# Kernel optimization log

Measured on AMD Instinct MI355X. Metric: run time of the kernel, lower is better.

The kernel has to match this reference:

```python
import jax, jax.numpy as jnp
import numpy as np

E = 256   # embedding_channels
C = 128   # c
N1 = 512
N2 = 512
NE1 = 16384
NE2 = 16384
EPS = 1e-5


def _ln(x, w, b):
    m = x.mean(-1, keepdims=True)
    v = jnp.mean((x - m) ** 2, axis=-1, keepdims=True)
    return (x - m) * jax.lax.rsqrt(v + EPS) * w + b


def _lin(x, w, b):
    return x @ w.T + b


def setup_inputs() -> dict:
    key = jax.random.key(0)
    ks = jax.random.split(key, 12)
    p = lambda k, shape: jax.random.normal(k, shape, jnp.float32) * 0.02
    return {
        "z": jax.random.normal(ks[0], (N1, N2, E), jnp.float32),
        "efeat1": jax.random.normal(ks[1], (NE1, E), jnp.float32),
        "efeat2": jax.random.normal(ks[2], (NE2, E), jnp.float32),
        "ln_w": jnp.ones((E,), jnp.float32), "ln_b": jnp.zeros((E,), jnp.float32),
        "lnc_w": jnp.ones((C,), jnp.float32), "lnc_b": jnp.zeros((C,), jnp.float32),
        "gl1_w": p(ks[3], (C, E)), "gl1_b": jnp.zeros((C,), jnp.float32),
        "gl2_w": p(ks[4], (C, E)), "gl2_b": jnp.zeros((C,), jnp.float32),
        "l1_w": p(ks[5], (C, E)), "l1_b": jnp.zeros((C,), jnp.float32),
        "l2_w": p(ks[6], (C, E)), "l2_b": jnp.zeros((C,), jnp.float32),
        "eg_w": p(ks[7], (E, E)), "eg_b": jnp.zeros((E,), jnp.float32),
        "las_w": p(ks[8], (E, C)), "las_b": jnp.zeros((E,), jnp.float32),
        "edges1": jax.random.randint(ks[9], (2, NE1), 0, N1, jnp.int64 if jax.config.jax_enable_x64 else jnp.int32),
        "edges2": jax.random.randint(ks[10], (2, NE2), 0, N2, jnp.int64 if jax.config.jax_enable_x64 else jnp.int32),
    }


def reference(z, efeat1, efeat2, ln_w, ln_b, lnc_w, lnc_b, gl1_w, gl1_b,
              gl2_w, gl2_b, l1_w, l1_b, l2_w, l2_b, eg_w, eg_b,
              las_w, las_b, edges1, edges2):
    zl = _ln(z, ln_w, ln_b)                       # [n1,n2,E]
    p1 = _ln(efeat1, ln_w, ln_b)                  # [ne1,E]
    p2 = _ln(efeat2, ln_w, ln_b)                  # [ne2,E]

    gate = lambda x, gw, gb, lw, lb: jax.nn.sigmoid(_lin(x, gw, gb)) * _lin(x, lw, lb)
    ab1 = gate(zl, gl1_w, gl1_b, l1_w, l1_b)      # [n1,n2,C]
    ab2 = gate(zl, gl2_w, gl2_b, l2_w, l2_b)      # [n1,n2,C]
    p1 = gate(p1, gl1_w, gl1_b, l1_w, l1_b)       # [ne1,C]
    p2 = gate(p2, gl2_w, gl2_b, l2_w, l2_b)       # [ne2,C]
    g = jax.nn.sigmoid(_lin(zl, eg_w, eg_b))      # [n1,n2,E]

    n1, n2 = z.shape[0], z.shape[1]
    # sparse COO -> dense (duplicate indices sum, matching torch coalesce)
    P1 = jnp.zeros((n1, n1, C), z.dtype).at[edges1[0], edges1[1]].add(p1)
    P2 = jnp.zeros((n2, n2, C), z.dtype).at[edges2[0], edges2[1]].add(p2)

    block1 = jnp.einsum('ikc,kjc->ijc', P1, ab1)  # [n1,n2,C]
    block2 = jnp.einsum('ikc,jkc->ijc', ab2, P2)  # [n1,n2,C]

    return g * _lin(_ln(block1 + block2, lnc_w, lnc_b), las_w, las_b)
```

## Files before the change

kernel.cpp:

```cpp
#include <hip/hip_runtime.h>
#include <stdint.h>

#define NN 512
#define EE 256
#define CC 128
#define NEDGE 16384
#define RR (NN*NN)
#define RT3 (RR + 2*NEDGE)

using bf16x8 = __attribute__((ext_vector_type(8))) short;
using f32x4  = __attribute__((ext_vector_type(4))) float;

__device__ __forceinline__ unsigned short f2bf(float f) {
  union { float f; unsigned u; } v; v.f = f;
  unsigned r = v.u + 0x7FFFu + ((v.u >> 16) & 1u);
  return (unsigned short)(r >> 16);
}
__device__ __forceinline__ float bf2f(unsigned short h) {
  union { unsigned u; float f; } v; v.u = ((unsigned)h) << 16;
  return v.f;
}
__device__ __forceinline__ float sigm(float x) { return 1.f / (1.f + __expf(-x)); }

__global__ __launch_bounds__(256) void k_ln(
    const float* __restrict__ z, const float* __restrict__ e1,
    const float* __restrict__ e2, const float* __restrict__ lnw,
    const float* __restrict__ lnb, unsigned short* __restrict__ zl) {
  int row = blockIdx.x * 4 + (threadIdx.x >> 6);
  int lane = threadIdx.x & 63;
  const float* src;
  if (row < RR)            src = z  + (size_t)row * EE;
  else if (row < RR+NEDGE) src = e1 + (size_t)(row - RR) * EE;
  else                     src = e2 + (size_t)(row - RR - NEDGE) * EE;
  float4 v = ((const float4*)src)[lane];
  float s = v.x + v.y + v.z + v.w;
  float q = v.x*v.x + v.y*v.y + v.z*v.z + v.w*v.w;
  #pragma unroll
  for (int o = 32; o > 0; o >>= 1) { s += __shfl_xor(s, o); q += __shfl_xor(q, o); }
  float m = s * (1.f/EE);
  float rstd = rsqrtf(q*(1.f/EE) - m*m + 1e-5f);
  float4 wv = ((const float4*)lnw)[lane];
  float4 bv = ((const float4*)lnb)[lane];
  ushort4 o4;
  o4.x = f2bf((v.x - m)*rstd*wv.x + bv.x);
  o4.y = f2bf((v.y - m)*rstd*wv.y + bv.y);
  o4.z = f2bf((v.z - m)*rstd*wv.z + bv.z);
  o4.w = f2bf((v.w - m)*rstd*wv.w + bv.w);
  ((ushort4*)(zl + (size_t)row * EE))[lane] = o4;
}

__global__ __launch_bounds__(256) void k_wconv(
    const float* __restrict__ gl1, const float* __restrict__ l1,
    const float* __restrict__ gl2, const float* __restrict__ l2,
    const float* __restrict__ eg,  const float* __restrict__ las,
    unsigned short* __restrict__ Wcol, unsigned short* __restrict__ Wrow,
    unsigned short* __restrict__ Wlas) {
  int t = blockIdx.x * 256 + threadIdx.x;
  if (t < 65536) {
    Wcol[t] = f2bf(t < 32768 ? gl1[t] : l1[t - 32768]);
  } else if (t < 196608) {
    int u = t - 65536;
    float v = (u < 32768) ? gl2[u] : (u < 65536) ? l2[u - 32768] : eg[u - 65536];
    Wrow[u] = f2bf(v);
  } else {
    int u = t - 196608;
    Wlas[u] = f2bf(las[u]);
  }
}

__global__ __launch_bounds__(256) void k_proj_gate(
    const unsigned short* __restrict__ zl, const unsigned short* __restrict__ W,
    const float* __restrict__ gb, const float* __restrict__ lb,
    unsigned short* __restrict__ abOut, float* __restrict__ Pf,
    const int* __restrict__ edges, int mode) {
  __shared__ __attribute__((aligned(16))) short As[128*32];
  __shared__ __attribute__((aligned(16))) short Bg[128*32];
  __shared__ __attribute__((aligned(16))) short Bl[128*32];
  const int t = threadIdx.x, w = t >> 6, lane = t & 63;
  const int mt = blockIdx.x;
  const bool isE = (mt >= RR/128);
  size_t abase; int astride;
  if (!isE) {
    if (mode == 0) { int rt0 = mt*128; abase = (size_t)(rt0 & 511)*512 + (rt0 >> 9); astride = 512; }
    else           { abase = (size_t)mt*128; astride = 1; }
  } else {
    abase = (size_t)RR + (mode ? NEDGE : 0) + (mt*128 - RR); astride = 1;
  }
  const f32x4 z4 = {0.f, 0.f, 0.f, 0.f};
  f32x4 ag[4][4], al[4][4];
  #pragma unroll
  for (int a = 0; a < 4; ++a)
    #pragma unroll
    for (int b = 0; b < 4; ++b) { ag[a][b] = z4; al[a][b] = z4; }
  const int wr = (w >> 1)*64, wc = (w & 1)*64;
  #pragma unroll 1
  for (int kk = 0; kk < 8; ++kk) {
    const int k0 = kk * 32;
    __syncthreads();
    #pragma unroll
    for (int s2 = 0; s2 < 2; ++s2) {
      int sidx = t + s2*256, row = sidx >> 2, seg = sidx & 3;
      int lo = row*32 + seg*8;
      *(uint4*)&As[lo] = *(const uint4*)(zl + (abase + (size_t)row*astride)*EE + k0 + seg*8);
      const unsigned short* wp = W + (size_t)row*EE + k0 + seg*8;
      *(uint4*)&Bg[lo] = *(const uint4*)wp;
      *(uint4*)&Bl[lo] = *(const uint4*)(wp + 128*EE);
    }
    __syncthreads();
    bf16x8 af[4], bgf[4], blf[4];
    #pragma unroll
    for (int f = 0; f < 4; ++f) {
      af[f]  = *(const bf16x8*)&As[(wr + f*16 + (lane & 15))*32 + (lane >> 4)*8];
      bgf[f] = *(const bf16x8*)&Bg[(wc + f*16 + (lane & 15))*32 + (lane >> 4)*8];
      blf[f] = *(const bf16x8*)&Bl[(wc + f*16 + (lane & 15))*32 + (lane >> 4)*8];
    }
    #pragma unroll
    for (int fm = 0; fm < 4; ++fm)
      #pragma unroll
      for (int fn = 0; fn < 4; ++fn) {
        ag[fm][fn] = __builtin_amdgcn_mfma_f32_16x16x32_bf16(af[fm], bgf[fn], ag[fm][fn], 0, 0, 0);
        al[fm][fn] = __builtin_amdgcn_mfma_f32_16x16x32_bf16(af[fm], blf[fn], al[fm][fn], 0, 0, 0);
      }
  }
  const int quad = lane >> 4, lc = lane & 15;
  #pragma unroll
  for (int fm = 0; fm < 4; ++fm)
    #pragma unroll
    for (int fn = 0; fn < 4; ++fn) {
      int c = wc + fn*16 + lc;
      float bgv = gb[c], blv = lb[c];
      float v0 = sigm(ag[fm][fn][0] + bgv) * (al[fm][fn][0] + blv);
      float v1 = sigm(ag[fm][fn][1] + bgv) * (al[fm][fn][1] + blv);
      float v2 = sigm(ag[fm][fn][2] + bgv) * (al[fm][fn][2] + blv);
      float v3 = sigm(ag[fm][fn][3] + bgv) * (al[fm][fn][3] + blv);
      int rl = wr + fm*16 + quad*4;
      if (!isE) {
        size_t rt = (size_t)mt*128 + rl;
        ushort4 o; o.x = f2bf(v0); o.y = f2bf(v1); o.z = f2bf(v2); o.w = f2bf(v3);
        *(ushort4*)&abOut[(size_t)c*RR + rt] = o;
      } else {
        int e0 = mt*128 - RR + rl;
        float vv[4] = {v0, v1, v2, v3};
        #pragma unroll
        for (int rg = 0; rg < 4; ++rg) {
          int e = e0 + rg;
          int i0 = edges[e], i1 = edges[NEDGE + e];
          atomicAdd(&Pf[((size_t)i0*NN + i1)*CC + c], vv[rg]);
        }
      }
    }
}

__global__ __launch_bounds__(256) void k_proj_g(
    const unsigned short* __restrict__ zl, const unsigned short* __restrict__ Weg,
    const float* __restrict__ egb, unsigned short* __restrict__ gOut) {
  __shared__ __attribute__((aligned(16))) short As[128*32];
  __shared__ __attribute__((aligned(16))) short Bs[128*32];
  const int t = threadIdx.x, w = t >> 6, lane = t & 63;
  const int mt = blockIdx.x, half = blockIdx.y;
  const size_t abase = (size_t)mt * 128;
  const unsigned short* Wb = Weg + (size_t)half * 128 * EE;
  const f32x4 z4 = {0.f, 0.f, 0.f, 0.f};
  f32x4 acc[4][4];
  #pragma unroll
  for (int a = 0; a < 4; ++a)
    #pragma unroll
    for (int b = 0; b < 4; ++b) acc[a][b] = z4;
  const int wr = (w >> 1)*64, wc = (w & 1)*64;
  #pragma unroll 1
  for (int kk = 0; kk < 8; ++kk) {
    const int k0 = kk * 32;
    __syncthreads();
    #pragma unroll
    for (int s2 = 0; s2 < 2; ++s2) {
      int sidx = t + s2*256, row = sidx >> 2, seg = sidx & 3;
      int lo = row*32 + seg*8;
      *(uint4*)&As[lo] = *(const uint4*)(zl + (abase + row)*EE + k0 + seg*8);
      *(uint4*)&Bs[lo] = *(const uint4*)(Wb + (size_t)row*EE + k0 + seg*8);
    }
    __syncthreads();
    bf16x8 af[4], bf_[4];
    #pragma unroll
    for (int f = 0; f < 4; ++f) {
      af[f]  = *(const bf16x8*)&As[(wr + f*16 + (lane & 15))*32 + (lane >> 4)*8];
      bf_[f] = *(const bf16x8*)&Bs[(wc + f*16 + (lane & 15))*32 + (lane >> 4)*8];
    }
    #pragma unroll
    for (int fm = 0; fm < 4; ++fm)
      #pragma unroll
      for (int fn = 0; fn < 4; ++fn)
        acc[fm][fn] = __builtin_amdgcn_mfma_f32_16x16x32_bf16(af[fm], bf_[fn], acc[fm][fn], 0, 0, 0);
  }
  const int quad = lane >> 4, lc = lane & 15;
  #pragma unroll
  for (int fm = 0; fm < 4; ++fm)
    #pragma unroll
    for (int fn = 0; fn < 4; ++fn) {
      int e = half*128 + wc + fn*16 + lc;
      float bv = egb[e];
      size_t r0 = (size_t)mt*128 + wr + fm*16 + quad*4;
      #pragma unroll
      for (int rg = 0; rg < 4; ++rg)
        gOut[(r0 + rg)*EE + e] = f2bf(sigm(acc[fm][fn][rg] + bv));
    }
}

__global__ __launch_bounds__(256) void k_pcvt(
    const float* __restrict__ P1f, const float* __restrict__ P2f,
    unsigned short* __restrict__ P1c, unsigned short* __restrict__ P2c) {
  const float* src = blockIdx.y ? P2f : P1f;
  unsigned short* dst = blockIdx.y ? P2c : P1c;
  __shared__ float Ls[128*65];
  const int t = threadIdx.x;
  const size_t pos0 = (size_t)blockIdx.x * 64;
  #pragma unroll
  for (int it = 0; it < 8; ++it) {
    int fi = t + it*256;
    int p = fi >> 5, cq = fi & 31;
    float4 v = ((const float4*)(src + (pos0 + p)*CC))[cq];
    Ls[(cq*4+0)*65 + p] = v.x; Ls[(cq*4+1)*65 + p] = v.y;
    Ls[(cq*4+2)*65 + p] = v.z; Ls[(cq*4+3)*65 + p] = v.w;
  }
  __syncthreads();
  #pragma unroll
  for (int it = 0; it < 8; ++it) {
    int oi = t + it*256;
    int c = oi >> 4, pq = oi & 15;
    ushort4 o;
    o.x = f2bf(Ls[c*65 + pq*4 + 0]); o.y = f2bf(Ls[c*65 + pq*4 + 1]);
    o.z = f2bf(Ls[c*65 + pq*4 + 2]); o.w = f2bf(Ls[c*65 + pq*4 + 3]);
    *(ushort4*)&dst[(size_t)c*RR + pos0 + pq*4] = o;
  }
}

__global__ __launch_bounds__(256) void k_einsum(
    const unsigned short* __restrict__ P1c, const unsigned short* __restrict__ ab1t,
    const unsigned short* __restrict__ ab2c, const unsigned short* __restrict__ P2c,
    float* __restrict__ Sf) {
  __shared__ __attribute__((aligned(16))) short A1s[128*32];
  __shared__ __attribute__((aligned(16))) short B1s[128*32];
  __shared__ __attribute__((aligned(16))) short A2s[128*32];
  __shared__ __attribute__((aligned(16))) short B2s[128*32];
  const int t = threadIdx.x, w = t >> 6, lane = t & 63;
  const int ch = blockIdx.y, mt = blockIdx.x & 3, nt = blockIdx.x >> 2;
  const size_t cb = (size_t)ch * RR;
  const unsigned short* A1g = P1c  + cb + (size_t)mt*128*512;
  const unsigned short* B1g = ab1t + cb + (size_t)nt*128*512;
  const unsigned short* A2g = ab2c + cb + (size_t)mt*128*512;
  const unsigned short* B2g = P2c  + cb + (size_t)nt*128*512;
  const f32x4 z4 = {0.f, 0.f, 0.f, 0.f};
  f32x4 acc[4][4];
  #pragma unroll
  for (int a = 0; a < 4; ++a)
    #pragma unroll
    for (int b = 0; b < 4; ++b) acc[a][b] = z4;
  const int wr = (w >> 1)*64, wc = (w & 1)*64;
  #pragma unroll 1
  for (int kk = 0; kk < 16; ++kk) {
    const int k0 = kk * 32;
    __syncthreads();
    #pragma unroll
    for (int s2 = 0; s2 < 2; ++s2) {
      int sidx = t + s2*256, row = sidx >> 2, seg = sidx & 3;
      int go = row*512 + k0 + seg*8;
      int lo = row*32 + seg*8;
      *(uint4*)&A1s[lo] = *(const uint4*)(A1g + go);
      *(uint4*)&B1s[lo] = *(const uint4*)(B1g + go);
      *(uint4*)&A2s[lo] = *(const uint4*)(A2g + go);
      *(uint4*)&B2s[lo] = *(const uint4*)(B2g + go);
    }
    __syncthreads();
    bf16x8 a1[4], b1[4], a2[4], b2[4];
    #pragma unroll
    for (int f = 0; f < 4; ++f) {
      int ro = (wr + f*16 + (lane & 15))*32 + (lane >> 4)*8;
      int co = (wc + f*16 + (lane & 15))*32 + (lane >> 4)*8;
      a1[f] = *(const bf16x8*)&A1s[ro];
      a2[f] = *(const bf16x8*)&A2s[ro];
      b1[f] = *(const bf16x8*)&B1s[co];
      b2[f] = *(const bf16x8*)&B2s[co];
    }
    #pragma unroll
    for (int fm = 0; fm < 4; ++fm)
      #pragma unroll
      for (int fn = 0; fn < 4; ++fn) {
        acc[fm][fn] = __builtin_amdgcn_mfma_f32_16x16x32_bf16(a1[fm], b1[fn], acc[fm][fn], 0, 0, 0);
        acc[fm][fn] = __builtin_amdgcn_mfma_f32_16x16x32_bf16(a2[fm], b2[fn], acc[fm][fn], 0, 0, 0);
      }
  }
  const int quad = lane >> 4, lc = lane & 15;
  #pragma unroll
  for (int fm = 0; fm < 4; ++fm)
    #pragma unroll
    for (int fn = 0; fn < 4; ++fn) {
      int j = nt*128 + wc + fn*16 + lc;
      int ib = mt*128 + wr + fm*16 + quad*4;
      #pragma unroll
      for (int rg = 0; rg < 4; ++rg)
        Sf[cb + (size_t)(ib + rg)*NN + j] = acc[fm][fn][rg];
    }
}

__global__ __launch_bounds__(256) void k_out(
    const float* __restrict__ Sf, const unsigned short* __restrict__ g,
    const unsigned short* __restrict__ Wlas, const float* __restrict__ lasb,
    const float* __restrict__ lncw, const float* __restrict__ lncb,
    float* __restrict__ out) {
  __shared__ float Sls[64*129];
  __shared__ __attribute__((aligned(16))) short Als[64*128];
  const int t = threadIdx.x, w = t >> 6, lane = t & 63;
  const size_t r0 = (size_t)blockIdx.x * 64;
  #pragma unroll
  for (int it = 0; it < 8; ++it) {
    int fi = t + it*256;
    int c = fi >> 4, rq = fi & 15;
    float4 v = ((const float4*)(Sf + (size_t)c*RR + r0))[rq];
    Sls[(rq*4+0)*129 + c] = v.x; Sls[(rq*4+1)*129 + c] = v.y;
    Sls[(rq*4+2)*129 + c] = v.z; Sls[(rq*4+3)*129 + c] = v.w;
  }
  __syncthreads();
  #pragma unroll 1
  for (int i = 0; i < 16; ++i) {
    int rr = w*16 + i;
    float x1 = Sls[rr*129 + lane], x2 = Sls[rr*129 + 64 + lane];
    float s = x1 + x2, q = x1*x1 + x2*x2;
    #pragma unroll
    for (int o = 32; o > 0; o >>= 1) { s += __shfl_xor(s, o); q += __shfl_xor(q, o); }
    float m = s * (1.f/CC);
    float rstd = rsqrtf(q*(1.f/CC) - m*m + 1e-5f);
    int c1 = lane, c2 = lane + 64;
    Als[rr*128 + c1] = (short)f2bf((x1 - m)*rstd*lncw[c1] + lncb[c1]);
    Als[rr*128 + c2] = (short)f2bf((x2 - m)*rstd*lncw[c2] + lncb[c2]);
  }
  __syncthreads();
  const f32x4 z4 = {0.f, 0.f, 0.f, 0.f};
  f32x4 acc[4][4];
  #pragma unroll
  for (int a = 0; a < 4; ++a)
    #pragma unroll
    for (int b = 0; b < 4; ++b) acc[a][b] = z4;
  const int quad = lane >> 4, lc = lane & 15;
  #pragma unroll
  for (int kk = 0; kk < 4; ++kk) {
    int k0 = kk * 32;
    bf16x8 a[4], b[4];
    #pragma unroll
    for (int f = 0; f < 4; ++f) {
      a[f] = *(const bf16x8*)&Als[(f*16 + lc)*128 + k0 + quad*8];
      int e = w*64 + f*16 + lc;
      b[f] = *(const bf16x8*)&Wlas[(size_t)e*CC + k0 + quad*8];
    }
    #pragma unroll
    for (int fm = 0; fm < 4; ++fm)
      #pragma unroll
      for (int fn = 0; fn < 4; ++fn)
        acc[fm][fn] = __builtin_amdgcn_mfma_f32_16x16x32_bf16(a[fm], b[fn], acc[fm][fn], 0, 0, 0);
  }
  #pragma unroll
  for (int fm = 0; fm < 4; ++fm)
    #pragma unroll
    for (int fn = 0; fn < 4; ++fn) {
      int e = w*64 + fn*16 + lc;
      float lbv = lasb[e];
      #pragma unroll
      for (int rg = 0; rg < 4; ++rg) {
        size_t r = r0 + fm*16 + quad*4 + rg;
        float gv = bf2f(g[r*EE + e]);
        out[r*EE + e] = gv * (acc[fm][fn][rg] + lbv);
      }
    }
}

extern "C" void kernel_launch(void* const* d_in, const int* in_sizes, int n_in,
                              void* d_out, int out_size, void* d_ws, size_t ws_size,
                              hipStream_t stream) {
  const float* z    = (const float*)d_in[0];
  const float* ef1  = (const float*)d_in[1];
  const float* ef2  = (const float*)d_in[2];
  const float* lnw  = (const float*)d_in[3];
  const float* lnb  = (const float*)d_in[4];
  const float* lncw = (const float*)d_in[5];
  const float* lncb = (const float*)d_in[6];
  const float* gl1w = (const float*)d_in[7];
  const float* gl1b = (const float*)d_in[8];
  const float* gl2w = (const float*)d_in[9];
  const float* gl2b = (const float*)d_in[10];
  const float* l1w  = (const float*)d_in[11];
  const float* l1b  = (const float*)d_in[12];
  const float* l2w  = (const float*)d_in[13];
  const float* l2b  = (const float*)d_in[14];
  const float* egw  = (const float*)d_in[15];
  const float* egb  = (const float*)d_in[16];
  const float* lasw = (const float*)d_in[17];
  const float* lasb = (const float*)d_in[18];
  const int* edges1 = (const int*)d_in[19];
  const int* edges2 = (const int*)d_in[20];
  float* out = (float*)d_out;

  char* ws = (char*)d_ws;
  unsigned short* zl   = (unsigned short*)(ws);
  unsigned short* P1c  = (unsigned short*)(ws);
  unsigned short* P2c  = (unsigned short*)(ws + 67108864);
  unsigned short* ab1t = (unsigned short*)(ws + 150994944);
  unsigned short* ab2c = (unsigned short*)(ws + 218103808);
  unsigned short* gbuf = (unsigned short*)(ws + 285212672);
  float* P1f = (float*)(ws + 419430400);
  float* Sf  = (float*)(ws + 419430400);
  float* P2f = (float*)(ws + 553648128);
  unsigned short* Wcol = (unsigned short*)(ws + 687865856);
  unsigned short* Wrow = (unsigned short*)(ws + 687996928);
  unsigned short* Wlas = (unsigned short*)(ws + 688259072);

  hipMemsetAsync(P1f, 0, (size_t)RR*CC*4, stream);
  hipMemsetAsync(P2f, 0, (size_t)RR*CC*4, stream);
  k_wconv<<<896, 256, 0, stream>>>(gl1w, l1w, gl2w, l2w, egw, lasw, Wcol, Wrow, Wlas);
  k_ln<<<RT3/4, 256, 0, stream>>>(z, ef1, ef2, lnw, lnb, zl);
  k_proj_gate<<<2176, 256, 0, stream>>>(zl, Wcol, gl1b, l1b, ab1t, P1f, edges1, 0);
  k_proj_gate<<<2176, 256, 0, stream>>>(zl, Wrow, gl2b, l2b, ab2c, P2f, edges2, 1);
  k_proj_g<<<dim3(2048, 2), 256, 0, stream>>>(zl, Wrow + 256*EE, egb, gbuf);
  k_pcvt<<<dim3(4096, 2), 256, 0, stream>>>(P1f, P2f, P1c, P2c);
  k_einsum<<<dim3(16, 128), 256, 0, stream>>>(P1c, ab1t, ab2c, P2c, Sf);
  k_out<<<4096, 256, 0, stream>>>(Sf, gbuf, Wlas, lasb, lncw, lncb, out);
}
```

Measured before the change: 1.355 ms.

## Swap MFMA operands for vector stores, XCD-aware einsum grid, restructure output LN

In k_proj_g and k_out the MFMA operands are swapped so each lane holds four consecutive output columns, which allows packed ushort4/float4 global stores and vector bias/gate loads in place of scalar ones. The einsum grid is flattened to 1D and remapped so consecutive blocks on the same XCD share a channel, aiming for better L2 reuse of the per-channel operands. k_out drops its padded transpose through LDS: each thread reads 32 strided channel values directly, reduces LayerNorm statistics with shuffles across four lanes, and writes into an XOR-swizzled LDS tile. The main risk is the strided per-thread global reads in k_out and higher register pressure from holding 32 floats per thread.

```diff
diff --git a/kernel.cpp b/kernel.cpp
--- a/kernel.cpp
+++ b/kernel.cpp
@@ -186,23 +186,27 @@
       bf_[f] = *(const bf16x8*)&Bs[(wc + f*16 + (lane & 15))*32 + (lane >> 4)*8];
     }
     #pragma unroll
-    for (int fm = 0; fm < 4; ++fm)
+    for (int fn = 0; fn < 4; ++fn)
       #pragma unroll
-      for (int fn = 0; fn < 4; ++fn)
-        acc[fm][fn] = __builtin_amdgcn_mfma_f32_16x16x32_bf16(af[fm], bf_[fn], acc[fm][fn], 0, 0, 0);
+      for (int fm = 0; fm < 4; ++fm)
+        acc[fn][fm] = __builtin_amdgcn_mfma_f32_16x16x32_bf16(bf_[fn], af[fm], acc[fn][fm], 0, 0, 0);
   }
   const int quad = lane >> 4, lc = lane & 15;
   #pragma unroll
-  for (int fm = 0; fm < 4; ++fm)
-    #pragma unroll
-    for (int fn = 0; fn < 4; ++fn) {
-      int e = half*128 + wc + fn*16 + lc;
-      float bv = egb[e];
-      size_t r0 = (size_t)mt*128 + wr + fm*16 + quad*4;
-      #pragma unroll
-      for (int rg = 0; rg < 4; ++rg)
-        gOut[(r0 + rg)*EE + e] = f2bf(sigm(acc[fm][fn][rg] + bv));
-    }
+  for (int fn = 0; fn < 4; ++fn) {
+    int e = half*128 + wc + fn*16 + quad*4;
+    float4 bv = *(const float4*)(egb + e);
+    #pragma unroll
+    for (int fm = 0; fm < 4; ++fm) {
+      size_t r = (size_t)mt*128 + wr + fm*16 + lc;
+      ushort4 o;
+      o.x = f2bf(sigm(acc[fn][fm][0] + bv.x));
+      o.y = f2bf(sigm(acc[fn][fm][1] + bv.y));
+      o.z = f2bf(sigm(acc[fn][fm][2] + bv.z));
+      o.w = f2bf(sigm(acc[fn][fm][3] + bv.w));
+      *(ushort4*)&gOut[r*EE + e] = o;
+    }
+  }
 }
 
 __global__ __launch_bounds__(256) void k_pcvt(
@@ -242,7 +246,11 @@
   __shared__ __attribute__((aligned(16))) short A2s[128*32];
   __shared__ __attribute__((aligned(16))) short B2s[128*32];
   const int t = threadIdx.x, w = t >> 6, lane = t & 63;
-  const int ch = blockIdx.y, mt = blockIdx.x & 3, nt = blockIdx.x >> 2;
+  const int n = blockIdx.x;
+  const int xcd = n & 7, bi = n >> 3;
+  const int ch = xcd * 16 + (bi >> 4);
+  const int tile = bi & 15;
+  const int mt = tile & 3, nt = tile >> 2;
   const size_t cb = (size_t)ch * RR;
   const unsigned short* A1g = P1c  + cb + (size_t)mt*128*512;
   const unsigned short* B1g = ab1t + cb + (size_t)nt*128*512;
@@ -306,69 +314,80 @@
     const unsigned short* __restrict__ Wlas, const float* __restrict__ lasb,
     const float* __restrict__ lncw, const float* __restrict__ lncb,
     float* __restrict__ out) {
-  __shared__ float Sls[64*129];
-  __shared__ __attribute__((aligned(16))) short Als[64*128];
+  __shared__ __attribute__((aligned(16))) char Als[64*256];
   const int t = threadIdx.x, w = t >> 6, lane = t & 63;
   const size_t r0 = (size_t)blockIdx.x * 64;
-  #pragma unroll
-  for (int it = 0; it < 8; ++it) {
-    int fi = t + it*256;
-    int c = fi >> 4, rq = fi & 15;
-    float4 v = ((const float4*)(Sf + (size_t)c*RR + r0))[rq];
-    Sls[(rq*4+0)*129 + c] = v.x; Sls[(rq*4+1)*129 + c] = v.y;
-    Sls[(rq*4+2)*129 + c] = v.z; Sls[(rq*4+3)*129 + c] = v.w;
+  const int row = t >> 2, part = t & 3;
+
+  float x[32];
+  const float* sp = Sf + (size_t)(part*32)*RR + r0 + row;
+  #pragma unroll
+  for (int i = 0; i < 32; ++i) x[i] = sp[(size_t)i*RR];
+  float s = 0.f, q = 0.f;
+  #pragma unroll
+  for (int i = 0; i < 32; ++i) { s += x[i]; q += x[i]*x[i]; }
+  s += __shfl_xor(s, 1); q += __shfl_xor(q, 1);
+  s += __shfl_xor(s, 2); q += __shfl_xor(q, 2);
+  float m = s * (1.f/CC);
+  float rstd = rsqrtf(q*(1.f/CC) - m*m + 1e-5f);
+
+  {
+    const float4* wv4 = (const float4*)(lncw + part*32);
+    const float4* bv4 = (const float4*)(lncb + part*32);
+    #pragma unroll
+    for (int i4 = 0; i4 < 8; ++i4) {
+      float4 wv = wv4[i4], bv = bv4[i4];
+      ushort4 o;
+      o.x = f2bf((x[i4*4+0]-m)*rstd*wv.x + bv.x);
+      o.y = f2bf((x[i4*4+1]-m)*rstd*wv.y + bv.y);
+      o.z = f2bf((x[i4*4+2]-m)*rstd*wv.z + bv.z);
+      o.w = f2bf((x[i4*4+3]-m)*rstd*wv.w + bv.w);
+      int boff = (part*64 + i4*8) ^ ((row & 7) << 4);
+      *(ushort4*)(Als + row*256 + boff) = o;
+    }
   }
   __syncthreads();
-  #pragma unroll 1
-  for (int i = 0; i < 16; ++i) {
-    int rr = w*16 + i;
-    float x1 = Sls[rr*129 + lane], x2 = Sls[rr*129 + 64 + lane];
-    float s = x1 + x2, q = x1*x1 + x2*x2;
-    #pragma unroll
-    for (int o = 32; o > 0; o >>= 1) { s += __shfl_xor(s, o); q += __shfl_xor(q, o); }
-    float m = s * (1.f/CC);
-    float rstd = rsqrtf(q*(1.f/CC) - m*m + 1e-5f);
-    int c1 = lane, c2 = lane + 64;
-    Als[rr*128 + c1] = (short)f2bf((x1 - m)*rstd*lncw[c1] + lncb[c1]);
-    Als[rr*128 + c2] = (short)f2bf((x2 - m)*rstd*lncw[c2] + lncb[c2]);
-  }
-  __syncthreads();
+
+  const int quad = lane >> 4, lc = lane & 15;
   const f32x4 z4 = {0.f, 0.f, 0.f, 0.f};
   f32x4 acc[4][4];
   #pragma unroll
   for (int a = 0; a < 4; ++a)
     #pragma unroll
     for (int b = 0; b < 4; ++b) acc[a][b] = z4;
-  const int quad = lane >> 4, lc = lane & 15;
   #pragma unroll
   for (int kk = 0; kk < 4; ++kk) {
-    int k0 = kk * 32;
-    bf16x8 a[4], b[4];
+    bf16x8 wf[4], sfr[4];
     #pragma unroll
     for (int f = 0; f < 4; ++f) {
-      a[f] = *(const bf16x8*)&Als[(f*16 + lc)*128 + k0 + quad*8];
-      int e = w*64 + f*16 + lc;
-      b[f] = *(const bf16x8*)&Wlas[(size_t)e*CC + k0 + quad*8];
-    }
-    #pragma unroll
-    for (int fm = 0; fm < 4; ++fm)
+      wf[f]  = *(const bf16x8*)(Wlas + (size_t)(w*64 + f*16 + lc)*CC + kk*32 + quad*8);
+      int r = f*16 + lc;
+      sfr[f] = *(const bf16x8*)(Als + r*256 + ((kk*64 + quad*16) ^ ((r & 7) << 4)));
+    }
+    #pragma unroll
+    for (int fe = 0; fe < 4; ++fe)
       #pragma unroll
-      for (int fn = 0; fn < 4; ++fn)
-        acc[fm][fn] = __builtin_amdgcn_mfma_f32_16x16x32_bf16(a[fm], b[fn], acc[fm][fn], 0, 0, 0);
-  }
-  #pragma unroll
-  for (int fm = 0; fm < 4; ++fm)
-    #pragma unroll
-    for (int fn = 0; fn < 4; ++fn) {
-      int e = w*64 + fn*16 + lc;
-      float lbv = lasb[e];
-      #pragma unroll
-      for (int rg = 0; rg < 4; ++rg) {
-        size_t r = r0 + fm*16 + quad*4 + rg;
-        float gv = bf2f(g[r*EE + e]);
-        out[r*EE + e] = gv * (acc[fm][fn][rg] + lbv);
-      }
-    }
+      for (int fr = 0; fr < 4; ++fr)
+        acc[fe][fr] = __builtin_amdgcn_mfma_f32_16x16x32_bf16(wf[fe], sfr[fr], acc[fe][fr], 0, 0, 0);
+  }
+
+  #pragma unroll
+  for (int fe = 0; fe < 4; ++fe) {
+    const int e0 = w*64 + fe*16 + quad*4;
+    const float4 lb = *(const float4*)(lasb + e0);
+    #pragma unroll
+    for (int fr = 0; fr < 4; ++fr) {
+      const size_t r = r0 + fr*16 + lc;
+      ushort4 gv = *(const ushort4*)(g + r*EE + e0);
+      f32x4 v = acc[fe][fr];
+      float4 o;
+      o.x = bf2f(gv.x) * (v[0] + lb.x);
+      o.y = bf2f(gv.y) * (v[1] + lb.y);
+      o.z = bf2f(gv.z) * (v[2] + lb.z);
+      o.w = bf2f(gv.w) * (v[3] + lb.w);
+      *(float4*)&out[r*EE + e0] = o;
+    }
+  }
 }
 
 extern "C" void kernel_launch(void* const* d_in, const int* in_sizes, int n_in,
@@ -419,6 +438,6 @@
   k_proj_gate<<<2176, 256, 0, stream>>>(zl, Wrow, gl2b, l2b, ab2c, P2f, edges2, 1);
   k_proj_g<<<dim3(2048, 2), 256, 0, stream>>>(zl, Wrow + 256*EE, egb, gbuf);
   k_pcvt<<<dim3(4096, 2), 256, 0, stream>>>(P1f, P2f, P1c, P2c);
-  k_einsum<<<dim3(16, 128), 256, 0, stream>>>(P1c, ab1t, ab2c, P2c, Sf);
+  k_einsum<<<2048, 256, 0, stream>>>(P1c, ab1t, ab2c, P2c, Sf);
   k_out<<<4096, 256, 0, stream>>>(Sf, gbuf, Wlas, lasb, lncw, lncb, out);
 }
```

Result: faster. 1.283 ms (-5.3%).
